# Kernel optimization log

Hardware: AMD Instinct MI355X
Metric: run time of the kernel (lower is better)

The kernel has to match this reference:

```python
import jax, jax.numpy as jnp
import numpy as np
import math

B, S, D, H, F, E, K, L, V = 1, 2048, 768, 12, 1536, 8, 2, 2, 32000


def _ln(x, w, b, eps=1e-5):
    m = x.mean(-1, keepdims=True)
    v = ((x - m) ** 2).mean(-1, keepdims=True)
    return (x - m) / jnp.sqrt(v + eps) * w + b


def setup_inputs() -> dict:
    key = jax.random.key(0)
    ks = jax.random.split(key, 16)
    std = 0.02
    inp = {
        'tokens': jax.random.randint(ks[0], (B, S), 0, V),
        'emb': jax.random.normal(ks[1], (V, D), jnp.float32) * std,
        'qkv_w': jax.random.normal(ks[2], (L, 3 * D, D), jnp.float32) * std,
        'qkv_b': jax.random.normal(ks[3], (L, 3 * D), jnp.float32) * std,
        'out_w': jax.random.normal(ks[4], (L, D, D), jnp.float32) * std,
        'out_b': jax.random.normal(ks[5], (L, D), jnp.float32) * std,
        'ln1_w': jnp.ones((L, D), jnp.float32),
        'ln1_b': jax.random.normal(ks[6], (L, D), jnp.float32) * std,
        'ln2_w': jnp.ones((L, D), jnp.float32),
        'ln2_b': jax.random.normal(ks[7], (L, D), jnp.float32) * std,
        'gate_w': jax.random.normal(ks[8], (L, E, D), jnp.float32) * std,
        'eg_w': jax.random.normal(ks[9], (L, E, F, D), jnp.float32) * std,
        'eu_w': jax.random.normal(ks[10], (L, E, F, D), jnp.float32) * std,
        'ed_w': jax.random.normal(ks[11], (L, E, D, F), jnp.float32) * std,
        'rms_w': jnp.ones((D,), jnp.float32),
    }
    return inp


def reference(tokens, emb, qkv_w, qkv_b, out_w, out_b, ln1_w, ln1_b,
              ln2_w, ln2_b, gate_w, eg_w, eu_w, ed_w, rms_w):
    Dh = D // H
    x = emb[tokens] * math.sqrt(D)  # (B,S,D)
    for l in range(L):
        # --- MultiheadAttention (batch_first, no mask, eval) ---
        qkv = x @ qkv_w[l].T + qkv_b[l]
        q, k, v = jnp.split(qkv, 3, axis=-1)
        q = q.reshape(B, S, H, Dh).transpose(0, 2, 1, 3)
        k = k.reshape(B, S, H, Dh).transpose(0, 2, 1, 3)
        v = v.reshape(B, S, H, Dh).transpose(0, 2, 1, 3)
        att = jax.nn.softmax(jnp.einsum('bhqd,bhkd->bhqk', q, k) / math.sqrt(Dh), axis=-1)
        o = jnp.einsum('bhqk,bhkd->bhqd', att, v).transpose(0, 2, 1, 3).reshape(B, S, D)
        o = o @ out_w[l].T + out_b[l]
        x = _ln(x + o, ln1_w[l], ln1_b[l])
        # --- SimpleDeepseekV3MoE: top-k gate, softmax over top-k scores ---
        gs = jnp.einsum('bsd,ed->bse', x, gate_w[l])
        topv, topi = jax.lax.top_k(gs, K)
        tw = jax.nn.softmax(topv, axis=-1)  # (B,S,K)
        # dense per-expert combine weight (0 for unselected experts)
        ew = jnp.sum(jax.nn.one_hot(topi, E, dtype=x.dtype) * tw[..., None], axis=-2)  # (B,S,E)
        hg = jax.nn.silu(jnp.einsum('bsd,efd->bsef', x, eg_w[l]))
        hu = jnp.einsum('bsd,efd->bsef', x, eu_w[l])
        ye = jnp.einsum('bsef,edf->bsed', hg * hu, ed_w[l])
        moe = jnp.einsum('bsed,bse->bsd', ye, ew)
        x = _ln(x + moe, ln2_w[l], ln2_b[l])
    # final RMSNorm (torch default eps=None -> finfo eps)
    rms = jnp.sqrt(jnp.mean(x * x, axis=-1, keepdims=True) + jnp.finfo(x.dtype).eps)
    x = x / rms * rms_w
    logits = x @ emb.T  # tied lm_head
    return logits
```

## Files before the change

kernel.cpp:

```cpp
#include <hip/hip_runtime.h>

#define SQ   2048
#define DM   768
#define NHD  12
#define DHD  64
#define FF   1536
#define NE   8
#define NL   2
#define NV   32000

typedef __attribute__((ext_vector_type(8))) short bf16x8;
typedef __attribute__((ext_vector_type(4))) float f32x4;

__device__ __forceinline__ unsigned short f2bf(float f) {
  unsigned u = __float_as_uint(f);
  return (unsigned short)((u + 0x7fffu + ((u >> 16) & 1u)) >> 16);
}
__device__ __forceinline__ float bf2f(unsigned short h) {
  return __uint_as_float(((unsigned)h) << 16);
}

#define GLD16(ldsp, gp) __builtin_amdgcn_global_load_lds( \
    (const __attribute__((address_space(1))) void*)(gp),  \
    (__attribute__((address_space(3))) void*)(ldsp), 16, 0, 0)

__device__ __forceinline__ void conv8(const float* s, unsigned short* d) {
  float4 a = *(const float4*)s;
  float4 b = *(const float4*)(s + 4);
  int4 pk = make_int4(
      (int)((unsigned)f2bf(a.x) | ((unsigned)f2bf(a.y) << 16)),
      (int)((unsigned)f2bf(a.z) | ((unsigned)f2bf(a.w) << 16)),
      (int)((unsigned)f2bf(b.x) | ((unsigned)f2bf(b.y) << 16)),
      (int)((unsigned)f2bf(b.z) | ((unsigned)f2bf(b.w) << 16)));
  *(int4*)d = pk;
}

__global__ __launch_bounds__(256) void conv_k(const float* __restrict__ s,
    unsigned short* __restrict__ d) {
  size_t i = (size_t)(blockIdx.x * 256 + threadIdx.x) * 8;
  conv8(s + i, d + i);
}

__global__ __launch_bounds__(256) void conv3_k(const float* __restrict__ s0,
    const float* __restrict__ s1, const float* __restrict__ s2,
    unsigned short* __restrict__ d, int per) {
  int b = blockIdx.x;
  const float* s = (b < per) ? s0 : (b < 2 * per) ? s1 : s2;
  int sb = (b < per) ? b : (b < 2 * per) ? b - per : b - 2 * per;
  size_t di = (size_t)b * 2048 + threadIdx.x * 8;
  size_t si = (size_t)sb * 2048 + threadIdx.x * 8;
  conv8(s + si, d + di);
}

__global__ __launch_bounds__(256) void conv2_k(const float* __restrict__ s0,
    const float* __restrict__ s1, unsigned short* __restrict__ d, int per0) {
  int b = blockIdx.x;
  const float* s = (b < per0) ? s0 : s1;
  int sb = (b < per0) ? b : b - per0;
  size_t di = (size_t)b * 2048 + threadIdx.x * 8;
  size_t si = (size_t)sb * 2048 + threadIdx.x * 8;
  conv8(s + si, d + di);
}

__global__ __launch_bounds__(256) void embed_k(const int* __restrict__ tok,
    const float* __restrict__ emb, float* __restrict__ x,
    unsigned short* __restrict__ xbf) {
  int idx = blockIdx.x * 256 + threadIdx.x;
  int s = idx / DM, d = idx % DM;
  float v = emb[(size_t)tok[s] * DM + d] * 27.712812921102035f;
  x[idx] = v;
  xbf[idx] = f2bf(v);
}

template<bool GATHER, bool OBF16>
__global__ __launch_bounds__(512) void gemm256_k(
    const unsigned short* __restrict__ A, long long lda,
    const unsigned short* __restrict__ B, long long ldb, long long b_z,
    void* __restrict__ C, long long ldc, long long c_z,
    int M, int Kd, int mT, int nT, int Z, int zmod,
    const int* __restrict__ glist, long long gl_z,
    const int* __restrict__ cnt)
{
  int nwg = gridDim.x, bid = blockIdx.x;
  int q = nwg >> 3, r = nwg & 7;
  int xcd = bid & 7, j = bid >> 3;
  int wid = (xcd < r ? xcd * (q + 1) : r * (q + 1) + (xcd - r) * q) + j;
  int z = wid % Z; int rem = wid / Z;
  int mt = rem % mT, nt = rem / mT;
  int zz = z % zmod;
  int Mz = cnt ? cnt[zz] : M;
  int m0 = mt * 128, n0 = nt * 256;
  if (m0 >= Mz) return;
  (void)nT;

  const unsigned short* Bz = B + (size_t)z * b_z;

  __shared__ __align__(16) unsigned short lds[3 * 6 * 4096];

  int t = threadIdx.x, w = t >> 6, lane = t & 63;
  int wm = (w >> 2) * 64, wn = (w & 3) * 64;
  int fr = lane & 15, ksg = lane >> 4;
  int lrow = lane >> 3;
  int lchunk = ((lane & 7) ^ lrow) * 8;

  const unsigned short* sp[6];
  #pragma unroll
  for (int hh = 0; hh < 2; ++hh) {
    int gr = m0 + hh * 64 + w * 8 + lrow; if (gr >= Mz) gr = Mz - 1;
    int arow;
    if constexpr (GATHER) arow = glist[(size_t)zz * gl_z + gr]; else arow = gr;
    sp[hh] = A + (size_t)arow * lda + lchunk;
  }
  #pragma unroll
  for (int hh = 0; hh < 4; ++hh)
    sp[2 + hh] = Bz + (size_t)(n0 + hh * 64 + w * 8 + lrow) * ldb + lchunk;

  int rdA = (w >> 2) * 4096;
  int rdB = (2 + (w & 3)) * 4096;
  int stDst = w * 512;

  int rx = fr & 7;
  int off0 = (ksg ^ rx) * 8;
  int off1 = ((4 + ksg) ^ rx) * 8;

  int KT = Kd >> 6;
  f32x4 acc[4][4] = {};

  #pragma unroll
  for (int h = 0; h < 6; ++h)
    GLD16(&lds[h * 4096 + stDst], sp[h]);
  #pragma unroll
  for (int h = 0; h < 6; ++h)
    GLD16(&lds[(6 + h) * 4096 + stDst], sp[h] + 64);
  asm volatile("s_waitcnt vmcnt(6)" ::: "memory");
  __builtin_amdgcn_s_barrier();
  __builtin_amdgcn_sched_barrier(0);

  int buf = 0;
  for (int kt = 0; kt < KT; ++kt) {
    const unsigned short* Abl = &lds[buf * 6 * 4096 + rdA];
    const unsigned short* Bbl = &lds[buf * 6 * 4096 + rdB];
    int pf = (kt + 2 < KT);
    int pbuf = buf + 2; if (pbuf >= 3) pbuf -= 3;
    unsigned short* pd = &lds[pbuf * 6 * 4096 + stDst];
    long long koff = (long long)(kt + 2) * 64;

    if (pf) {
      GLD16(pd + 0 * 4096, sp[0] + koff);
      GLD16(pd + 1 * 4096, sp[1] + koff);
      GLD16(pd + 2 * 4096, sp[2] + koff);
    }
    {
      bf16x8 af[4], bv[4];
      #pragma unroll
      for (int m = 0; m < 4; ++m)
        af[m] = *(const bf16x8*)&Abl[(m * 16 + fr) * 64 + off0];
      #pragma unroll
      for (int n = 0; n < 4; ++n)
        bv[n] = *(const bf16x8*)&Bbl[(n * 16 + fr) * 64 + off0];
      __builtin_amdgcn_s_setprio(1);
      #pragma unroll
      for (int m = 0; m < 4; ++m)
        #pragma unroll
        for (int n = 0; n < 4; ++n)
          acc[m][n] = __builtin_amdgcn_mfma_f32_16x16x32_bf16(
              af[m], bv[n], acc[m][n], 0, 0, 0);
      __builtin_amdgcn_s_setprio(0);
    }
    if (pf) {
      GLD16(pd + 3 * 4096, sp[3] + koff);
      GLD16(pd + 4 * 4096, sp[4] + koff);
      GLD16(pd + 5 * 4096, sp[5] + koff);
    }
    {
      bf16x8 af[4], bv[4];
      #pragma unroll
      for (int m = 0; m < 4; ++m)
        af[m] = *(const bf16x8*)&Abl[(m * 16 + fr) * 64 + off1];
      #pragma unroll
      for (int n = 0; n < 4; ++n)
        bv[n] = *(const bf16x8*)&Bbl[(n * 16 + fr) * 64 + off1];
      __builtin_amdgcn_s_setprio(1);
      #pragma unroll
      for (int m = 0; m < 4; ++m)
        #pragma unroll
        for (int n = 0; n < 4; ++n)
          acc[m][n] = __builtin_amdgcn_mfma_f32_16x16x32_bf16(
              af[m], bv[n], acc[m][n], 0, 0, 0);
      __builtin_amdgcn_s_setprio(0);
    }
    if (pf) {
      asm volatile("s_waitcnt vmcnt(6)" ::: "memory");
    } else if (kt + 1 < KT) {
      asm volatile("s_waitcnt vmcnt(0)" ::: "memory");
    }
    __builtin_amdgcn_s_barrier();
    __builtin_amdgcn_sched_barrier(0);
    buf = buf + 1; if (buf == 3) buf = 0;
  }

  int rb = ksg * 4;
  #pragma unroll
  for (int m = 0; m < 4; ++m) {
    #pragma unroll
    for (int n = 0; n < 4; ++n) {
      #pragma unroll
      for (int rr = 0; rr < 4; ++rr) {
        int row = m0 + wm + m * 16 + rb + rr;
        if (row >= Mz) continue;
        size_t off = (size_t)z * c_z + (size_t)row * ldc +
                     (n0 + wn + n * 16 + fr);
        if constexpr (OBF16) ((unsigned short*)C)[off] = f2bf(acc[m][n][rr]);
        else                 ((float*)C)[off] = acc[m][n][rr];
      }
    }
  }
}

template<bool GATHER, bool BIAS, bool OBF16>
__global__ __launch_bounds__(256) void gemm_k(
    const unsigned short* __restrict__ A, long long lda, long long a_z,
    const unsigned short* __restrict__ B, long long ldb, long long b_z,
    const float* __restrict__ bias,
    void* __restrict__ C, long long ldc, long long c_z,
    int M, int N, int Kd, float scale,
    const int* __restrict__ glist, long long gl_z,
    const int* __restrict__ cnt, int mT, int nT, int Z)
{
  int nwg = gridDim.x, bid = blockIdx.x;
  int q = nwg >> 3, r = nwg & 7;
  int xcd = bid & 7, j = bid >> 3;
  int wid = (xcd < r ? xcd * (q + 1) : r * (q + 1) + (xcd - r) * q) + j;
  int z = wid % Z; int rem = wid / Z;
  int mt = rem % mT, nt = rem / mT;

  int Mz = cnt ? cnt[z] : M;
  int m0 = mt * 128, n0 = nt * 128;
  if (m0 >= Mz) return;

  const unsigned short* Ab = A + (size_t)z * a_z;
  const unsigned short* Bb = B + (size_t)z * b_z;

  __shared__ __align__(16) unsigned short As[128 * 64];
  __shared__ __align__(16) unsigned short Bs[128 * 64];

  int t = threadIdx.x, w = t >> 6, lane = t & 63;
  int wm = (w >> 1) * 64, wn = (w & 1) * 64;
  int fr = lane & 15, ksg = lane >> 4;
  int lrow = lane >> 3;
  int lchunk = ((lane & 7) ^ lrow) * 8;

  const unsigned short* ap[4];
  const unsigned short* bp[4];
  unsigned short* la[4];
  unsigned short* lb[4];
  #pragma unroll
  for (int i = 0; i < 4; ++i) {
    int rrow = w * 32 + i * 8 + lrow;
    int gr = m0 + rrow; if (gr >= Mz) gr = Mz - 1;
    int arow; if constexpr (GATHER) arow = glist[(size_t)z * gl_z + gr]; else arow = gr;
    ap[i] = Ab + (size_t)arow * lda + lchunk;
    int br = n0 + rrow; if (br >= N) br = N - 1;
    bp[i] = Bb + (size_t)br * ldb + lchunk;
    la[i] = &As[(w * 32 + i * 8) * 64];
    lb[i] = &Bs[(w * 32 + i * 8) * 64];
  }

  int rx = fr & 7;
  int off0 = ((0 + ksg) ^ rx) * 8;
  int off1 = ((4 + ksg) ^ rx) * 8;

  f32x4 acc[4][4] = {};

  for (int k0 = 0; k0 < Kd; k0 += 64) {
    #pragma unroll
    for (int i = 0; i < 4; ++i) GLD16(la[i], ap[i] + k0);
    #pragma unroll
    for (int i = 0; i < 4; ++i) GLD16(lb[i], bp[i] + k0);
    __syncthreads();
    #pragma unroll
    for (int kb = 0; kb < 2; ++kb) {
      int offk = kb ? off1 : off0;
      bf16x8 af[4], bv[4];
      #pragma unroll
      for (int m = 0; m < 4; ++m)
        af[m] = *(const bf16x8*)&As[(wm + m * 16 + fr) * 64 + offk];
      #pragma unroll
      for (int n = 0; n < 4; ++n)
        bv[n] = *(const bf16x8*)&Bs[(wn + n * 16 + fr) * 64 + offk];
      #pragma unroll
      for (int m = 0; m < 4; ++m)
        #pragma unroll
        for (int n = 0; n < 4; ++n)
          acc[m][n] = __builtin_amdgcn_mfma_f32_16x16x32_bf16(
              af[m], bv[n], acc[m][n], 0, 0, 0);
    }
    __syncthreads();
  }

  int rb = ksg * 4;
  #pragma unroll
  for (int m = 0; m < 4; ++m) {
    #pragma unroll
    for (int n = 0; n < 4; ++n) {
      int col = n0 + wn + n * 16 + fr;
      if (col >= N) continue;
      #pragma unroll
      for (int rr = 0; rr < 4; ++rr) {
        int row = m0 + wm + m * 16 + rb + rr;
        if (row >= Mz) continue;
        float v = acc[m][n][rr] * scale;
        if constexpr (BIAS) v += bias[col];
        size_t off = (size_t)z * c_z + (size_t)row * ldc + col;
        if constexpr (OBF16) ((unsigned short*)C)[off] = f2bf(v);
        else                 ((float*)C)[off] = v;
      }
    }
  }
}

__global__ __launch_bounds__(256) void transpose_v_k(
    const unsigned short* __restrict__ qkv, unsigned short* __restrict__ vt) {
  int kt = blockIdx.x;
  int h  = blockIdx.y;
  __shared__ unsigned short tile[64][72];
  int t = threadIdx.x;
  int r = t >> 2;
  int c0 = (t & 3) * 16;
  const unsigned short* src =
      qkv + (size_t)(kt * 64 + r) * (3 * DM) + 2 * DM + h * DHD + c0;
  *(int4*)&tile[r][c0]     = *(const int4*)(src);
  *(int4*)&tile[r][c0 + 8] = *(const int4*)(src + 8);
  __syncthreads();
  unsigned u[8];
  #pragma unroll
  for (int j = 0; j < 8; ++j)
    u[j] = (unsigned)tile[c0 + 2 * j][r] | ((unsigned)tile[c0 + 2 * j + 1][r] << 16);
  unsigned short* dst = vt + (size_t)(h * DHD + r) * SQ + kt * 64 + c0;
  *(int4*)dst       = make_int4((int)u[0], (int)u[1], (int)u[2], (int)u[3]);
  *(int4*)(dst + 8) = make_int4((int)u[4], (int)u[5], (int)u[6], (int)u[7]);
}

__global__ __launch_bounds__(128) void flash_k(
    const unsigned short* __restrict__ qkv,
    const unsigned short* __restrict__ vt,
    unsigned short* __restrict__ o)
{
  int nwg = gridDim.x, bid = blockIdx.x;
  int cpx = nwg >> 3;
  int wid = (bid & 7) * cpx + (bid >> 3);
  int h  = wid >> 6;
  int qt = wid & 63;
  int q0 = qt * 32;

  __shared__ __align__(16) unsigned short Ks[128 * 64];
  __shared__ __align__(16) unsigned short Vs[128 * 64];
  __shared__ __align__(16) unsigned short Ps[2][16 * 136];

  int t = threadIdx.x, w = t >> 6, lane = t & 63;
  int fr = lane & 15, ksg = lane >> 4;
  int lrow = lane >> 3;
  int lchunk = ((lane & 7) ^ lrow) * 8;

  const unsigned short* qbase = qkv + (size_t)q0 * (3 * DM) + h * DHD;
  #pragma unroll
  for (int i = 0; i < 2; ++i) {
    int rrow = w * 16 + i * 8 + lrow;
    GLD16(&Ks[(w * 16 + i * 8) * 64], qbase + (size_t)rrow * (3 * DM) + lchunk);
  }
  __syncthreads();
  bf16x8 qf[2];
  {
    int row = w * 16 + fr, ph = fr & 7;
    qf[0] = *(const bf16x8*)&Ks[row * 64 + ((ksg ^ ph) * 8)];
    qf[1] = *(const bf16x8*)&Ks[row * 64 + (((4 + ksg) ^ ph) * 8)];
  }
  __syncthreads();

  const unsigned short* kbase = qkv + DM + h * DHD;
  const unsigned short* vb = vt + (size_t)(h * DHD) * SQ;

  f32x4 oacc[4] = {};
  float m_r[4] = {-1e30f, -1e30f, -1e30f, -1e30f};
  float l_r[4] = {0.f, 0.f, 0.f, 0.f};

  for (int kt = 0; kt < SQ / 128; ++kt) {
    int kk0 = kt * 128;
    #pragma unroll
    for (int i = 0; i < 8; ++i) {
      int rrow = w * 64 + i * 8 + lrow;
      GLD16(&Ks[(w * 64 + i * 8) * 64],
            kbase + (size_t)(kk0 + rrow) * (3 * DM) + lchunk);
    }
    #pragma unroll
    for (int i = 0; i < 8; ++i) {
      int p = w * 64 + i * 8 + lrow;
      GLD16(&Vs[(w * 64 + i * 8) * 64],
            vb + (size_t)(p >> 1) * SQ + kk0 + (p & 1) * 64 + lchunk);
    }
    __syncthreads();

    f32x4 sacc[8] = {};
    #pragma unroll
    for (int kb = 0; kb < 2; ++kb) {
      #pragma unroll
      for (int n = 0; n < 8; ++n) {
        int row = n * 16 + fr;
        bf16x8 bvv = *(const bf16x8*)&Ks[row * 64 +
            (((kb * 4 + ksg) ^ (fr & 7)) * 8)];
        sacc[n] = __builtin_amdgcn_mfma_f32_16x16x32_bf16(
            qf[kb], bvv, sacc[n], 0, 0, 0);
      }
    }

    #pragma unroll
    for (int r = 0; r < 4; ++r) {
      float mx = sacc[0][r];
      #pragma unroll
      for (int n = 1; n < 8; ++n) mx = fmaxf(mx, sacc[n][r]);
      mx = fmaxf(mx, __shfl_xor(mx, 1));
      mx = fmaxf(mx, __shfl_xor(mx, 2));
      mx = fmaxf(mx, __shfl_xor(mx, 4));
      mx = fmaxf(mx, __shfl_xor(mx, 8));
      float mn = fmaxf(m_r[r], mx * 0.125f);
      float resc = __expf(m_r[r] - mn);
      m_r[r] = mn;
      #pragma unroll
      for (int n = 0; n < 4; ++n) oacc[n][r] *= resc;
      float rs = 0.f;
      #pragma unroll
      for (int n = 0; n < 8; ++n) {
        float p = __expf(sacc[n][r] * 0.125f - mn);
        rs += p;
        Ps[w][(ksg * 4 + r) * 136 + n * 16 + fr] = f2bf(p);
      }
      rs += __shfl_xor(rs, 1);
      rs += __shfl_xor(rs, 2);
      rs += __shfl_xor(rs, 4);
      rs += __shfl_xor(rs, 8);
      l_r[r] = l_r[r] * resc + rs;
    }

    #pragma unroll
    for (int ksi = 0; ksi < 4; ++ksi) {
      bf16x8 pa = *(const bf16x8*)&Ps[w][fr * 136 + ksi * 32 + ksg * 8];
      #pragma unroll
      for (int n = 0; n < 4; ++n) {
        int p = (n * 16 + fr) * 2 + (ksi >> 1);
        int c = (ksi & 1) * 4 + ksg;
        bf16x8 bvv = *(const bf16x8*)&Vs[p * 64 + ((c ^ (p & 7)) * 8)];
        oacc[n] = __builtin_amdgcn_mfma_f32_16x16x32_bf16(
            pa, bvv, oacc[n], 0, 0, 0);
      }
    }
    __syncthreads();
  }

  unsigned short* ob = o + (size_t)(q0 + w * 16) * DM + h * DHD;
  #pragma unroll
  for (int r = 0; r < 4; ++r) {
    float invl = 1.f / l_r[r];
    int qrow = ksg * 4 + r;
    #pragma unroll
    for (int n = 0; n < 4; ++n)
      ob[(size_t)qrow * DM + n * 16 + fr] = f2bf(oacc[n][r] * invl);
  }
}

__global__ __launch_bounds__(256) void add_ln_k(const float* __restrict__ xin,
    const float* __restrict__ add, const float* __restrict__ w,
    const float* __restrict__ b, float* __restrict__ xout,
    unsigned short* __restrict__ xbf) {
  int row = blockIdx.x, t = threadIdx.x;
  const float* xi = xin + (size_t)row * DM;
  const float* ai = add + (size_t)row * DM;
  float v[3]; float s = 0.f, sq = 0.f;
  #pragma unroll
  for (int i = 0; i < 3; ++i) {
    int idx = t + i * 256;
    v[i] = xi[idx] + ai[idx];
    s += v[i]; sq += v[i] * v[i];
  }
  #pragma unroll
  for (int o = 32; o; o >>= 1) { s += __shfl_xor(s, o); sq += __shfl_xor(sq, o); }
  __shared__ float rsm[4], rqm[4];
  int wv = t >> 6;
  if ((t & 63) == 0) { rsm[wv] = s; rqm[wv] = sq; }
  __syncthreads();
  s = rsm[0] + rsm[1] + rsm[2] + rsm[3];
  sq = rqm[0] + rqm[1] + rqm[2] + rqm[3];
  float mean = s * (1.f / 768.f);
  float var = sq * (1.f / 768.f) - mean * mean;
  float inv = rsqrtf(var + 1e-5f);
  float* xo = xout + (size_t)row * DM;
  unsigned short* xb = xbf + (size_t)row * DM;
  #pragma unroll
  for (int i = 0; i < 3; ++i) {
    int idx = t + i * 256;
    float y = (v[i] - mean) * inv * w[idx] + b[idx];
    xo[idx] = y; xb[idx] = f2bf(y);
  }
}

__global__ void gate_topk_k(const float* __restrict__ x, const float* __restrict__ gw,
    float* __restrict__ tw, int* __restrict__ ti, int* __restrict__ cnt,
    int* __restrict__ lists, int* __restrict__ slot) {
  int sIdx = blockIdx.x, lane = threadIdx.x;
  const float* xr = x + (size_t)sIdx * DM;
  float acc[NE] = {};
  for (int d = lane; d < DM; d += 64) {
    float xv = xr[d];
    #pragma unroll
    for (int e = 0; e < NE; ++e) acc[e] += xv * gw[e * DM + d];
  }
  #pragma unroll
  for (int e = 0; e < NE; ++e) {
    #pragma unroll
    for (int o = 32; o; o >>= 1) acc[e] += __shfl_down(acc[e], o);
  }
  if (lane == 0) {
    float v0 = -1e30f, v1 = -1e30f; int i0 = 0, i1 = 0;
    #pragma unroll
    for (int e = 0; e < NE; ++e) {
      float v = acc[e];
      if (v > v0) { v1 = v0; i1 = i0; v0 = v; i0 = e; }
      else if (v > v1) { v1 = v; i1 = e; }
    }
    float e1 = expf(v1 - v0);
    float inv = 1.f / (1.f + e1);
    tw[sIdx * 2] = inv; tw[sIdx * 2 + 1] = e1 * inv;
    ti[sIdx * 2] = i0;  ti[sIdx * 2 + 1] = i1;
    int p0 = atomicAdd(&cnt[i0], 1); lists[i0 * SQ + p0] = sIdx; slot[sIdx * 2] = p0;
    int p1 = atomicAdd(&cnt[i1], 1); lists[i1 * SQ + p1] = sIdx; slot[sIdx * 2 + 1] = p1;
  }
}

__global__ void zero_k(int* __restrict__ c) {
  if (threadIdx.x < NE) c[threadIdx.x] = 0;
}

__global__ __launch_bounds__(256) void silu_mul_k(unsigned short* __restrict__ hg,
    const unsigned short* __restrict__ hu, const int* __restrict__ cnt) {
  int e = blockIdx.y, sl = blockIdx.x;
  if (sl >= cnt[e]) return;
  size_t base = ((size_t)e * SQ + sl) * FF;
  int t = threadIdx.x;
  #pragma unroll
  for (int i = 0; i < FF / 256; ++i) {
    size_t idx = base + t + i * 256;
    float g = bf2f(hg[idx]);
    float u = bf2f(hu[idx]);
    float sv = g / (1.f + expf(-g));
    hg[idx] = f2bf(sv * u);
  }
}

__global__ __launch_bounds__(256) void combine_ln_k(const float* __restrict__ xin,
    const float* __restrict__ ye, const float* __restrict__ tw,
    const int* __restrict__ ti, const int* __restrict__ slot,
    const float* __restrict__ w, const float* __restrict__ b,
    float* __restrict__ xout, unsigned short* __restrict__ xbf) {
  int row = blockIdx.x, t = threadIdx.x;
  int e0 = ti[row * 2], e1 = ti[row * 2 + 1];
  int p0 = slot[row * 2], p1 = slot[row * 2 + 1];
  float w0 = tw[row * 2], w1 = tw[row * 2 + 1];
  const float* y0 = ye + ((size_t)e0 * SQ + p0) * DM;
  const float* y1 = ye + ((size_t)e1 * SQ + p1) * DM;
  const float* xi = xin + (size_t)row * DM;
  float v[3]; float s = 0.f, sq = 0.f;
  #pragma unroll
  for (int i = 0; i < 3; ++i) {
    int idx = t + i * 256;
    v[i] = xi[idx] + w0 * y0[idx] + w1 * y1[idx];
    s += v[i]; sq += v[i] * v[i];
  }
  #pragma unroll
  for (int o = 32; o; o >>= 1) { s += __shfl_xor(s, o); sq += __shfl_xor(sq, o); }
  __shared__ float rsm[4], rqm[4];
  int wv = t >> 6;
  if ((t & 63) == 0) { rsm[wv] = s; rqm[wv] = sq; }
  __syncthreads();
  s = rsm[0] + rsm[1] + rsm[2] + rsm[3];
  sq = rqm[0] + rqm[1] + rqm[2] + rqm[3];
  float mean = s * (1.f / 768.f);
  float var = sq * (1.f / 768.f) - mean * mean;
  float inv = rsqrtf(var + 1e-5f);
  float* xo = xout + (size_t)row * DM;
  unsigned short* xb = xbf + (size_t)row * DM;
  #pragma unroll
  for (int i = 0; i < 3; ++i) {
    int idx = t + i * 256;
    float y = (v[i] - mean) * inv * w[idx] + b[idx];
    xo[idx] = y; xb[idx] = f2bf(y);
  }
}

__global__ __launch_bounds__(256) void rms_k(const float* __restrict__ x,
    const float* __restrict__ rw, unsigned short* __restrict__ xbf) {
  int row = blockIdx.x, t = threadIdx.x;
  const float* xi = x + (size_t)row * DM;
  float v[3]; float sq = 0.f;
  #pragma unroll
  for (int i = 0; i < 3; ++i) {
    int idx = t + i * 256;
    v[i] = xi[idx];
    sq += v[i] * v[i];
  }
  #pragma unroll
  for (int o = 32; o; o >>= 1) sq += __shfl_xor(sq, o);
  __shared__ float rqm[4];
  int wv = t >> 6;
  if ((t & 63) == 0) rqm[wv] = sq;
  __syncthreads();
  sq = rqm[0] + rqm[1] + rqm[2] + rqm[3];
  float inv = rsqrtf(sq * (1.f / 768.f) + 1.1920929e-07f);
  unsigned short* xb = xbf + (size_t)row * DM;
  #pragma unroll
  for (int i = 0; i < 3; ++i) {
    int idx = t + i * 256;
    xb[idx] = f2bf(v[i] * inv * rw[idx]);
  }
}

extern "C" void kernel_launch(void* const* d_in, const int* in_sizes, int n_in,
                              void* d_out, int out_size, void* d_ws, size_t ws_size,
                              hipStream_t stream) {
  (void)in_sizes; (void)n_in; (void)out_size; (void)ws_size;
  const int*   tokens = (const int*)d_in[0];
  const float* emb    = (const float*)d_in[1];
  const float* qkv_w  = (const float*)d_in[2];
  const float* qkv_b  = (const float*)d_in[3];
  const float* out_w  = (const float*)d_in[4];
  const float* out_b  = (const float*)d_in[5];
  const float* ln1_w  = (const float*)d_in[6];
  const float* ln1_b  = (const float*)d_in[7];
  const float* ln2_w  = (const float*)d_in[8];
  const float* ln2_b  = (const float*)d_in[9];
  const float* gate_w = (const float*)d_in[10];
  const float* eg_w   = (const float*)d_in[11];
  const float* eu_w   = (const float*)d_in[12];
  const float* ed_w   = (const float*)d_in[13];
  const float* rms_w  = (const float*)d_in[14];
  float* out = (float*)d_out;

  char* wsb = (char*)d_ws;
  float*          x_f    = (float*)(wsb + 0);
  unsigned short* x_bf   = (unsigned short*)(wsb + 6291456);
  unsigned short* qkv_bf = (unsigned short*)(wsb + 9437184);
  unsigned short* vt     = (unsigned short*)(wsb + 18874368);
  unsigned short* o_bf   = (unsigned short*)(wsb + 22020096);
  float*          tmp_f  = (float*)(wsb + 25165824);
  float*          tw     = (float*)(wsb + 31457280);
  int*            ti     = (int*)(wsb + 31473664);
  int*            cnt    = (int*)(wsb + 31490048);
  int*            lists  = (int*)(wsb + 31490304);
  int*            slot   = (int*)(wsb + 31555840);
  unsigned short* emb_bf = (unsigned short*)(wsb + 31572224);
  unsigned short* wbf    = (unsigned short*)(wsb + 80724224);
  unsigned short* hg     = (unsigned short*)(wsb + 142065920);
  unsigned short* hu     = (unsigned short*)(wsb + 142065920 + 50331648);
  float*          ye     = (float*)(wsb + 142065920 + 50331648);

  unsigned short* qw_bf = wbf;
  unsigned short* ow_bf = wbf + 1769472;
  unsigned short* eg_bf = wbf + 2359296;
  unsigned short* eu_bf = wbf + 11796480;
  unsigned short* ed_bf = wbf + 21233664;

  conv_k<<<12000, 256, 0, stream>>>(emb, emb_bf);
  embed_k<<<SQ * DM / 256, 256, 0, stream>>>(tokens, emb, x_f, x_bf);

  for (int l = 0; l < NL; ++l) {
    const float* qw = qkv_w + (size_t)l * 3 * DM * DM;
    const float* qb = qkv_b + (size_t)l * 3 * DM;
    const float* ob = out_b + (size_t)l * DM;
    const float* ow = out_w + (size_t)l * DM * DM;
    const float* gw = gate_w + (size_t)l * NE * DM;
    const float* egw = eg_w + (size_t)l * NE * FF * DM;
    const float* euw = eu_w + (size_t)l * NE * FF * DM;
    const float* edw = ed_w + (size_t)l * NE * DM * FF;

    conv2_k<<<1152, 256, 0, stream>>>(qw, ow, qw_bf, 864);
    conv3_k<<<13824, 256, 0, stream>>>(egw, euw, edw, eg_bf, 4608);

    gemm_k<false, true, true><<<16 * 18, 256, 0, stream>>>(
        x_bf, DM, 0, qw_bf, DM, 0, qb, qkv_bf, 3 * DM, 0,
        SQ, 3 * DM, DM, 1.f, nullptr, 0, nullptr, 16, 18, 1);

    transpose_v_k<<<dim3(SQ / 64, NHD), 256, 0, stream>>>(qkv_bf, vt);

    flash_k<<<NHD * 64, 128, 0, stream>>>(qkv_bf, vt, o_bf);

    gemm_k<false, true, false><<<16 * 6, 256, 0, stream>>>(
        o_bf, DM, 0, ow_bf, DM, 0, ob, tmp_f, DM, 0,
        SQ, DM, DM, 1.f, nullptr, 0, nullptr, 16, 6, 1);

    add_ln_k<<<SQ, 256, 0, stream>>>(x_f, tmp_f, ln1_w + l * DM, ln1_b + l * DM,
                                     x_f, x_bf);

    zero_k<<<1, 64, 0, stream>>>(cnt);
    gate_topk_k<<<SQ, 64, 0, stream>>>(x_f, gw, tw, ti, cnt, lists, slot);

    gemm256_k<true, true><<<16 * 6 * 16, 512, 0, stream>>>(
        x_bf, DM, eg_bf, DM, (long long)FF * DM,
        hg, FF, (long long)SQ * FF,
        SQ, DM, 16, 6, 16, 8, lists, SQ, cnt);

    silu_mul_k<<<dim3(SQ, NE), 256, 0, stream>>>(hg, hu, cnt);

    gemm_k<false, false, false><<<16 * 6 * NE, 256, 0, stream>>>(
        hg, FF, (long long)SQ * FF, ed_bf, FF, (long long)DM * FF, nullptr,
        ye, DM, (long long)SQ * DM,
        SQ, DM, FF, 1.f, nullptr, 0, cnt, 16, 6, NE);

    combine_ln_k<<<SQ, 256, 0, stream>>>(x_f, ye, tw, ti, slot,
                                         ln2_w + l * DM, ln2_b + l * DM,
                                         x_f, x_bf);
  }

  rms_k<<<SQ, 256, 0, stream>>>(x_f, rms_w, x_bf);

  gemm256_k<false, false><<<16 * 125, 512, 0, stream>>>(
      x_bf, DM, emb_bf, DM, 0, out, NV, 0,
      SQ, DM, 16, 125, 1, 1, nullptr, 0, nullptr);
}
```

Baseline: 813.1 us.

## Add dedicated 256x256-tile ping-pong GEMM kernel for tied LM head

```diff
diff --git a/kernel.cpp b/kernel.cpp
--- a/kernel.cpp
+++ b/kernel.cpp
@@ -70,6 +70,146 @@
   float v = emb[(size_t)tok[s] * DM + d] * 27.712812921102035f;
   x[idx] = v;
   xbf[idx] = f2bf(v);
+}
+
+__global__ __launch_bounds__(512, 2) void gemm8p_k(
+    const unsigned short* __restrict__ A, long long lda,
+    const unsigned short* __restrict__ B, long long ldb,
+    float* __restrict__ C, long long ldc,
+    int Kd, int mT)
+{
+  int nwg = gridDim.x, bid = blockIdx.x;
+  int q = nwg >> 3, r = nwg & 7;
+  int xcd = bid & 7, j = bid >> 3;
+  int wid = (xcd < r ? xcd * (q + 1) : r * (q + 1) + (xcd - r) * q) + j;
+  int mt = wid % mT, nt = wid / mT;
+  int m0 = mt * 256, n0 = nt * 256;
+
+  __shared__ __align__(16) unsigned short lds[2][2][16384];
+
+  int t = threadIdx.x, w = t >> 6, lane = t & 63;
+  int wm = w >> 2, wn = w & 3;
+  int fr = lane & 15, ksg = lane >> 4;
+
+  int srow = t >> 3;
+  int schunk = ((t & 7) ^ (srow & 7)) * 8;
+  const unsigned short* sa[4];
+  const unsigned short* sb[4];
+  #pragma unroll
+  for (int i = 0; i < 4; ++i) {
+    sa[i] = A + (size_t)(m0 + i * 64 + srow) * lda + schunk;
+    sb[i] = B + (size_t)(n0 + i * 64 + srow) * ldb + schunk;
+  }
+
+  int KT = Kd >> 6;
+  f32x4 acc[8][4] = {};
+
+#define STAGE_A(bufi, k0) { \
+    _Pragma("unroll") \
+    for (int i = 0; i < 4; ++i) \
+      GLD16(&lds[bufi][0][(i * 64 + w * 8) * 64], sa[i] + (k0)); }
+#define STAGE_B(bufi, k0) { \
+    _Pragma("unroll") \
+    for (int i = 0; i < 4; ++i) \
+      GLD16(&lds[bufi][1][(i * 64 + w * 8) * 64], sb[i] + (k0)); }
+#define MFMA16(MQ) { \
+    _Pragma("unroll") \
+    for (int m = 0; m < 4; ++m) \
+      _Pragma("unroll") \
+      for (int n = 0; n < 4; ++n) \
+        acc[(MQ) * 4 + m][n] = __builtin_amdgcn_mfma_f32_16x16x32_bf16( \
+            afr[m], bfr[n], acc[(MQ) * 4 + m][n], 0, 0, 0); }
+
+  STAGE_A(0, 0); STAGE_B(0, 0);
+  asm volatile("s_waitcnt vmcnt(0)" ::: "memory");
+  __builtin_amdgcn_s_barrier();
+  __builtin_amdgcn_sched_barrier(0);
+
+  int buf = 0;
+  for (int kt = 0; kt < KT; ++kt) {
+    const unsigned short* Al = &lds[buf][0][0];
+    const unsigned short* Bl = &lds[buf][1][0];
+    int pf = (kt + 1 < KT);
+    long long koff = (long long)(kt + 1) * 64;
+    bf16x8 bfr[4], afr[4];
+
+    {
+      int ko = ((0 + ksg) ^ (fr & 7)) * 8;
+      #pragma unroll
+      for (int n = 0; n < 4; ++n)
+        bfr[n] = *(const bf16x8*)&Bl[(wn * 64 + n * 16 + fr) * 64 + ko];
+      #pragma unroll
+      for (int m = 0; m < 4; ++m)
+        afr[m] = *(const bf16x8*)&Al[(wm * 128 + m * 16 + fr) * 64 + ko];
+      if (pf) STAGE_A(buf ^ 1, koff);
+      __builtin_amdgcn_s_barrier();
+      asm volatile("s_waitcnt lgkmcnt(0)" ::: "memory");
+      __builtin_amdgcn_sched_barrier(0);
+      __builtin_amdgcn_s_setprio(1);
+      MFMA16(0);
+      __builtin_amdgcn_s_setprio(0);
+      __builtin_amdgcn_s_barrier();
+    }
+    {
+      int ko = ((0 + ksg) ^ (fr & 7)) * 8;
+      #pragma unroll
+      for (int m = 0; m < 4; ++m)
+        afr[m] = *(const bf16x8*)&Al[(wm * 128 + 64 + m * 16 + fr) * 64 + ko];
+      if (pf) STAGE_B(buf ^ 1, koff);
+      __builtin_amdgcn_s_barrier();
+      asm volatile("s_waitcnt lgkmcnt(0)" ::: "memory");
+      __builtin_amdgcn_sched_barrier(0);
+      __builtin_amdgcn_s_setprio(1);
+      MFMA16(1);
+      __builtin_amdgcn_s_setprio(0);
+      __builtin_amdgcn_s_barrier();
+    }
+    {
+      int ko = ((4 + ksg) ^ (fr & 7)) * 8;
+      #pragma unroll
+      for (int n = 0; n < 4; ++n)
+        bfr[n] = *(const bf16x8*)&Bl[(wn * 64 + n * 16 + fr) * 64 + ko];
+      #pragma unroll
+      for (int m = 0; m < 4; ++m)
+        afr[m] = *(const bf16x8*)&Al[(wm * 128 + m * 16 + fr) * 64 + ko];
+      __builtin_amdgcn_s_barrier();
+      asm volatile("s_waitcnt lgkmcnt(0)" ::: "memory");
+      __builtin_amdgcn_sched_barrier(0);
+      __builtin_amdgcn_s_setprio(1);
+      MFMA16(0);
+      __builtin_amdgcn_s_setprio(0);
+      __builtin_amdgcn_s_barrier();
+    }
+    {
+      int ko = ((4 + ksg) ^ (fr & 7)) * 8;
+      #pragma unroll
+      for (int m = 0; m < 4; ++m)
+        afr[m] = *(const bf16x8*)&Al[(wm * 128 + 64 + m * 16 + fr) * 64 + ko];
+      __builtin_amdgcn_s_barrier();
+      asm volatile("s_waitcnt lgkmcnt(0)" ::: "memory");
+      __builtin_amdgcn_sched_barrier(0);
+      __builtin_amdgcn_s_setprio(1);
+      MFMA16(1);
+      __builtin_amdgcn_s_setprio(0);
+      if (pf) asm volatile("s_waitcnt vmcnt(0)" ::: "memory");
+      __builtin_amdgcn_s_barrier();
+      __builtin_amdgcn_sched_barrier(0);
+    }
+    buf ^= 1;
+  }
+#undef STAGE_A
+#undef STAGE_B
+#undef MFMA16
+
+  int rb = ksg * 4;
+  #pragma unroll
+  for (int M = 0; M < 8; ++M)
+    #pragma unroll
+    for (int n = 0; n < 4; ++n)
+      #pragma unroll
+      for (int rr = 0; rr < 4; ++rr)
+        C[(size_t)(m0 + wm * 128 + M * 16 + rb + rr) * ldc +
+          (n0 + wn * 64 + n * 16 + fr)] = acc[M][n][rr];
 }
 
 template<bool GATHER, bool OBF16>
@@ -664,7 +804,6 @@
   unsigned short* qw_bf = wbf;
   unsigned short* ow_bf = wbf + 1769472;
   unsigned short* eg_bf = wbf + 2359296;
-  unsigned short* eu_bf = wbf + 11796480;
   unsigned short* ed_bf = wbf + 21233664;
 
   conv_k<<<12000, 256, 0, stream>>>(emb, emb_bf);
@@ -720,7 +859,6 @@
 
   rms_k<<<SQ, 256, 0, stream>>>(x_f, rms_w, x_bf);
 
-  gemm256_k<false, false><<<16 * 125, 512, 0, stream>>>(
-      x_bf, DM, emb_bf, DM, 0, out, NV, 0,
-      SQ, DM, 16, 125, 1, 1, nullptr, 0, nullptr);
-}
+  gemm8p_k<<<8 * 125, 512, 0, stream>>>(
+      x_bf, DM, emb_bf, DM, out, NV, DM, 8);
+}
```

Result: no change. 801.0 us (-1.5%).
